# Optimization experiments

Measured on AMD Instinct MI355X. Metric: run time of the kernel, lower is better.

## Reference

```python
import jax, jax.numpy as jnp
import numpy as np

N = 4096

def setup_inputs() -> dict:
    key = jax.random.key(0)
    kA, kB = jax.random.split(key)
    # A and B are upper-triangular inputs, as the module assumes
    A = jnp.triu(jax.random.normal(kA, (N, N), dtype=jnp.float32))
    B = jnp.triu(jax.random.normal(kB, (N, N), dtype=jnp.float32))
    return {"A": A, "B": B}

def reference(A, B):
    # C = triu(A @ B); product of upper-triangular matrices is upper-triangular,
    # the kernel additionally masks the lower triangle of the output.
    return jnp.triu(A @ B)
```

## Files before the change

### kernel.cpp

```cpp
#include <hip/hip_runtime.h>


#define N   4096
#define NB  32
#define BM  128
#define PK  64
#define CH  8
#define NWG 1000
#define RS  72

typedef __attribute__((ext_vector_type(8))) __bf16 bf16x8;
typedef __attribute__((ext_vector_type(4))) float  floatx4;
typedef __attribute__((ext_vector_type(8))) unsigned short ushort8;

__device__ __forceinline__ unsigned short f32_to_bf16_rne(float f) {
    unsigned u = __builtin_bit_cast(unsigned, f);
    unsigned r = u + 0x7fffu + ((u >> 16) & 1u);
    return (unsigned short)(r >> 16);
}

__global__ __launch_bounds__(256)
void prep_kernel(const float* __restrict__ A, const float* __restrict__ B,
                 unsigned short* __restrict__ Ab, unsigned short* __restrict__ Bt,
                 float* __restrict__ C) {
    __shared__ float tile[64][65];
    const int bx = blockIdx.x, by = blockIdx.y;
    const int x0 = bx * 64, y0 = by * 64;
    const int xb = bx >> 1, yb = by >> 1;
    const int t  = threadIdx.x;
    const int tr = t >> 2, tc = (t & 3) * 16;

    if (xb >= yb) {
        const float* src = A + (size_t)(y0 + tr) * N + x0 + tc;
        const float4 v0 = ((const float4*)src)[0];
        const float4 v1 = ((const float4*)src)[1];
        const float4 v2 = ((const float4*)src)[2];
        const float4 v3 = ((const float4*)src)[3];
        ushort8 o0, o1;
        o0[0]=f32_to_bf16_rne(v0.x); o0[1]=f32_to_bf16_rne(v0.y);
        o0[2]=f32_to_bf16_rne(v0.z); o0[3]=f32_to_bf16_rne(v0.w);
        o0[4]=f32_to_bf16_rne(v1.x); o0[5]=f32_to_bf16_rne(v1.y);
        o0[6]=f32_to_bf16_rne(v1.z); o0[7]=f32_to_bf16_rne(v1.w);
        o1[0]=f32_to_bf16_rne(v2.x); o1[1]=f32_to_bf16_rne(v2.y);
        o1[2]=f32_to_bf16_rne(v2.z); o1[3]=f32_to_bf16_rne(v2.w);
        o1[4]=f32_to_bf16_rne(v3.x); o1[5]=f32_to_bf16_rne(v3.y);
        o1[6]=f32_to_bf16_rne(v3.z); o1[7]=f32_to_bf16_rne(v3.w);
        unsigned short* dst = Ab + (size_t)(y0 + tr) * N + x0 + tc;
        ((ushort8*)dst)[0] = o0;
        ((ushort8*)dst)[1] = o1;
    }
    if (xb <= yb) {
        const float* src = B + (size_t)(x0 + tr) * N + y0 + tc;
        const float4 v0 = ((const float4*)src)[0];
        const float4 v1 = ((const float4*)src)[1];
        const float4 v2 = ((const float4*)src)[2];
        const float4 v3 = ((const float4*)src)[3];
        float* d = &tile[tr][tc];
        d[0]=v0.x; d[1]=v0.y; d[2]=v0.z; d[3]=v0.w;
        d[4]=v1.x; d[5]=v1.y; d[6]=v1.z; d[7]=v1.w;
        d[8]=v2.x; d[9]=v2.y; d[10]=v2.z; d[11]=v2.w;
        d[12]=v3.x; d[13]=v3.y; d[14]=v3.z; d[15]=v3.w;
        __syncthreads();
        ushort8 o0, o1;
        #pragma unroll
        for (int i = 0; i < 8; ++i) o0[i] = f32_to_bf16_rne(tile[tc + i][tr]);
        #pragma unroll
        for (int i = 0; i < 8; ++i) o1[i] = f32_to_bf16_rne(tile[tc + 8 + i][tr]);
        unsigned short* dst = Bt + (size_t)(y0 + tr) * N + x0 + tc;
        ((ushort8*)dst)[0] = o0;
        ((ushort8*)dst)[1] = o1;
    }
    if (xb < yb || (xb - yb) >= CH) {
        float4 z = {0.f, 0.f, 0.f, 0.f};
        float* dst = C + (size_t)(y0 + tr) * N + x0 + tc;
        ((float4*)dst)[0] = z; ((float4*)dst)[1] = z;
        ((float4*)dst)[2] = z; ((float4*)dst)[3] = z;
    }
}

__global__ __launch_bounds__(256, 2)
void trimm_kernel(const unsigned short* __restrict__ Ab,
                  const unsigned short* __restrict__ Bt,
                  float* __restrict__ C) {
    __shared__ unsigned short sA[2][BM * RS];
    __shared__ unsigned short sB[2][BM * RS];

    int rem = blockIdx.x;
    int d = 0, per = 1;
    for (int dd = NB - 1; dd >= 0; --dd) {
        const int p   = (dd + CH) / CH;
        const int cnt = (NB - dd) * p;
        if (rem < cnt) { d = dd; per = p; break; }
        rem -= cnt;
    }
    const int tile  = rem / per;
    const int chunk = rem - tile * per;
    const int bi = tile, bj = tile + d;
    const int c    = d + 1;
    const int base = c / per, extra = c - base * per;
    const int kb0  = bi + chunk * base + (chunk < extra ? chunk : extra);
    const int len  = base + (chunk < extra ? 1 : 0);

    const int tid  = threadIdx.x;
    const int w    = tid >> 6;
    const int lane = tid & 63;
    const int quad = lane >> 4;
    const int l15  = lane & 15;

    const int m0 = (w >> 1) * 64;
    const int n0 = (w & 1) * 64;
    const int row0 = bi * BM;
    const int col0 = bj * BM;

    floatx4 acc[4][4] = {};

    const int srow8 = lane >> 3;
    const int sk    = (lane & 7) * 8;
    int lofs[4];
    const unsigned short* gA[4];
    const unsigned short* gB[4];
    #pragma unroll
    for (int i = 0; i < 4; ++i) {
        const int r = w * 32 + i * 8 + srow8;
        lofs[i] = r * RS + sk;
        gA[i] = Ab + (size_t)(row0 + r) * N + kb0 * BM + sk;
        gB[i] = Bt + (size_t)(col0 + r) * N + kb0 * BM + sk;
    }

    const int np = len * 2;

    ushort8 aR[4], bR[4];
    #pragma unroll
    for (int i = 0; i < 4; ++i) { aR[i] = *(const ushort8*)gA[i]; gA[i] += PK; }
    #pragma unroll
    for (int i = 0; i < 4; ++i) { bR[i] = *(const ushort8*)gB[i]; gB[i] += PK; }

    auto compute_phase = [&](int buf) {
        #pragma unroll
        for (int h = 0; h < 2; ++h) {
            bf16x8 af[4], bfr[4];
            #pragma unroll
            for (int t = 0; t < 4; ++t) {
                af[t]  = *(const bf16x8*)&sA[buf][(m0 + t * 16 + l15) * RS + h * 32 + quad * 8];
                bfr[t] = *(const bf16x8*)&sB[buf][(n0 + t * 16 + l15) * RS + h * 32 + quad * 8];
            }
            #pragma unroll
            for (int tm = 0; tm < 4; ++tm)
                #pragma unroll
                for (int tn = 0; tn < 4; ++tn)
                    acc[tm][tn] = __builtin_amdgcn_mfma_f32_16x16x32_bf16(
                        af[tm], bfr[tn], acc[tm][tn], 0, 0, 0);
        }
    };

    for (int p = 0; p < np - 1; ++p) {
        const int buf = p & 1;
        #pragma unroll
        for (int i = 0; i < 4; ++i) *(ushort8*)&sA[buf][lofs[i]] = aR[i];
        #pragma unroll
        for (int i = 0; i < 4; ++i) *(ushort8*)&sB[buf][lofs[i]] = bR[i];
        __syncthreads();
        #pragma unroll
        for (int i = 0; i < 4; ++i) { aR[i] = *(const ushort8*)gA[i]; gA[i] += PK; }
        #pragma unroll
        for (int i = 0; i < 4; ++i) { bR[i] = *(const ushort8*)gB[i]; gB[i] += PK; }
        compute_phase(buf);
    }
    {
        const int buf = (np - 1) & 1;
        #pragma unroll
        for (int i = 0; i < 4; ++i) *(ushort8*)&sA[buf][lofs[i]] = aR[i];
        #pragma unroll
        for (int i = 0; i < 4; ++i) *(ushort8*)&sB[buf][lofs[i]] = bR[i];
        __syncthreads();
        compute_phase(buf);
    }

    #pragma unroll
    for (int tm = 0; tm < 4; ++tm) {
        const int grow_base = row0 + m0 + tm * 16 + quad * 4;
        #pragma unroll
        for (int tn = 0; tn < 4; ++tn) {
            const int gcol = col0 + n0 + tn * 16 + l15;
            #pragma unroll
            for (int r = 0; r < 4; ++r) {
                const int grow = grow_base + r;
                float* p = C + (size_t)grow * N + gcol;
                const float v = acc[tm][tn][r];
                if (per > 1) {
                    atomicAdd(p, v);
                } else if (d != 0) {
                    *p = v;
                } else {
                    *p = (gcol >= grow) ? v : 0.0f;
                }
            }
        }
    }
}

extern "C" void kernel_launch(void* const* d_in, const int* in_sizes, int n_in,
                              void* d_out, int out_size, void* d_ws, size_t ws_size,
                              hipStream_t stream) {
    const float* A = (const float*)d_in[0];
    const float* B = (const float*)d_in[1];
    float* C = (float*)d_out;

    unsigned short* Ab = (unsigned short*)d_ws;
    unsigned short* Bt = Ab + (size_t)N * N;

    prep_kernel<<<dim3(N / 64, N / 64), dim3(256), 0, stream>>>(A, B, Ab, Bt, C);
    trimm_kernel<<<dim3(NWG), dim3(256), 0, stream>>>(Ab, Bt, C);
}
```

Before: 234.7 us.

## Replace split-K atomic scheduling with persistent snake-ordered full-K tile jobs

The kernel no longer splits the K range of long off-diagonal tiles across workgroups with atomicAdd accumulation. Instead it launches 512 persistent workgroups that walk the 528 upper-triangular output tiles in snake order, each computing its full K range and storing results directly. The prep kernel no longer pre-zeroes the output tiles that were accumulated with atomics. This removes the atomic traffic and the extra zeroing, but the longest tiles now run 32 K-blocks serially in a single workgroup, which risks severe load imbalance on the critical path.

```diff
diff --git a/kernel.cpp b/kernel.cpp
--- a/kernel.cpp
+++ b/kernel.cpp
@@ -1,13 +1,13 @@
 #include <hip/hip_runtime.h>
 
 
-#define N   4096
-#define NB  32
-#define BM  128
-#define PK  64
-#define CH  8
-#define NWG 1000
-#define RS  72
+#define N    4096
+#define NB   32
+#define BM   128
+#define PK   64
+#define NWG  512
+#define NJOB 528
+#define RS   72
 
 typedef __attribute__((ext_vector_type(8))) __bf16 bf16x8;
 typedef __attribute__((ext_vector_type(4))) float  floatx4;
@@ -70,7 +70,7 @@
         ((ushort8*)dst)[0] = o0;
         ((ushort8*)dst)[1] = o1;
     }
-    if (xb < yb || (xb - yb) >= CH) {
+    if (xb < yb) {
         float4 z = {0.f, 0.f, 0.f, 0.f};
         float* dst = C + (size_t)(y0 + tr) * N + x0 + tc;
         ((float4*)dst)[0] = z; ((float4*)dst)[1] = z;
@@ -85,22 +85,6 @@
     __shared__ unsigned short sA[2][BM * RS];
     __shared__ unsigned short sB[2][BM * RS];
 
-    int rem = blockIdx.x;
-    int d = 0, per = 1;
-    for (int dd = NB - 1; dd >= 0; --dd) {
-        const int p   = (dd + CH) / CH;
-        const int cnt = (NB - dd) * p;
-        if (rem < cnt) { d = dd; per = p; break; }
-        rem -= cnt;
-    }
-    const int tile  = rem / per;
-    const int chunk = rem - tile * per;
-    const int bi = tile, bj = tile + d;
-    const int c    = d + 1;
-    const int base = c / per, extra = c - base * per;
-    const int kb0  = bi + chunk * base + (chunk < extra ? chunk : extra);
-    const int len  = base + (chunk < extra ? 1 : 0);
-
     const int tid  = threadIdx.x;
     const int w    = tid >> 6;
     const int lane = tid & 63;
@@ -109,90 +93,116 @@
 
     const int m0 = (w >> 1) * 64;
     const int n0 = (w & 1) * 64;
-    const int row0 = bi * BM;
-    const int col0 = bj * BM;
-
-    floatx4 acc[4][4] = {};
 
     const int srow8 = lane >> 3;
     const int sk    = (lane & 7) * 8;
-    int lofs[4];
-    const unsigned short* gA[4];
-    const unsigned short* gB[4];
+    int lofs[4], rr[4];
     #pragma unroll
     for (int i = 0; i < 4; ++i) {
-        const int r = w * 32 + i * 8 + srow8;
-        lofs[i] = r * RS + sk;
-        gA[i] = Ab + (size_t)(row0 + r) * N + kb0 * BM + sk;
-        gB[i] = Bt + (size_t)(col0 + r) * N + kb0 * BM + sk;
-    }
-
-    const int np = len * 2;
-
-    ushort8 aR[4], bR[4];
-    #pragma unroll
-    for (int i = 0; i < 4; ++i) { aR[i] = *(const ushort8*)gA[i]; gA[i] += PK; }
-    #pragma unroll
-    for (int i = 0; i < 4; ++i) { bR[i] = *(const ushort8*)gB[i]; gB[i] += PK; }
-
-    auto compute_phase = [&](int buf) {
-        #pragma unroll
-        for (int h = 0; h < 2; ++h) {
-            bf16x8 af[4], bfr[4];
-            #pragma unroll
-            for (int t = 0; t < 4; ++t) {
-                af[t]  = *(const bf16x8*)&sA[buf][(m0 + t * 16 + l15) * RS + h * 32 + quad * 8];
-                bfr[t] = *(const bf16x8*)&sB[buf][(n0 + t * 16 + l15) * RS + h * 32 + quad * 8];
+        rr[i]   = w * 32 + i * 8 + srow8;
+        lofs[i] = rr[i] * RS + sk;
+    }
+
+    for (int p = 0;; ++p) {
+        const int idx = p * NWG + ((p & 1) ? (NWG - 1 - (int)blockIdx.x)
+                                           : (int)blockIdx.x);
+        if (idx >= NJOB) break;
+
+        int rem = idx, d = NB - 1;
+        for (; d >= 0; --d) {
+            const int cnt = NB - d;
+            if (rem < cnt) break;
+            rem -= cnt;
+        }
+        const int bi = rem, bj = bi + d;
+        const int row0 = bi * BM;
+        const int col0 = bj * BM;
+
+        floatx4 acc[4][4] = {};
+
+        const unsigned short* gA[4];
+        const unsigned short* gB[4];
+        #pragma unroll
+        for (int i = 0; i < 4; ++i) {
+            gA[i] = Ab + (size_t)(row0 + rr[i]) * N + bi * BM + sk;
+            gB[i] = Bt + (size_t)(col0 + rr[i]) * N + bi * BM + sk;
+        }
+
+        const int np = (d + 1) * 2;
+
+        ushort8 aR[4], bR[4];
+        #pragma unroll
+        for (int i = 0; i < 4; ++i) { aR[i] = *(const ushort8*)gA[i]; gA[i] += PK; }
+        #pragma unroll
+        for (int i = 0; i < 4; ++i) { bR[i] = *(const ushort8*)gB[i]; gB[i] += PK; }
+
+        for (int ph = 0; ph < np - 1; ++ph) {
+            const int buf = ph & 1;
+            #pragma unroll
+            for (int i = 0; i < 4; ++i) *(ushort8*)&sA[buf][lofs[i]] = aR[i];
+            #pragma unroll
+            for (int i = 0; i < 4; ++i) *(ushort8*)&sB[buf][lofs[i]] = bR[i];
+            __syncthreads();
+            #pragma unroll
+            for (int i = 0; i < 4; ++i) { aR[i] = *(const ushort8*)gA[i]; gA[i] += PK; }
+            #pragma unroll
+            for (int i = 0; i < 4; ++i) { bR[i] = *(const ushort8*)gB[i]; gB[i] += PK; }
+            #pragma unroll
+            for (int h = 0; h < 2; ++h) {
+                bf16x8 af[4], bfr[4];
+                #pragma unroll
+                for (int t = 0; t < 4; ++t) {
+                    af[t]  = *(const bf16x8*)&sA[buf][(m0 + t * 16 + l15) * RS + h * 32 + quad * 8];
+                    bfr[t] = *(const bf16x8*)&sB[buf][(n0 + t * 16 + l15) * RS + h * 32 + quad * 8];
+                }
+                #pragma unroll
+                for (int tm = 0; tm < 4; ++tm)
+                    #pragma unroll
+                    for (int tn = 0; tn < 4; ++tn)
+                        acc[tm][tn] = __builtin_amdgcn_mfma_f32_16x16x32_bf16(
+                            af[tm], bfr[tn], acc[tm][tn], 0, 0, 0);
             }
-            #pragma unroll
-            for (int tm = 0; tm < 4; ++tm)
-                #pragma unroll
-                for (int tn = 0; tn < 4; ++tn)
-                    acc[tm][tn] = __builtin_amdgcn_mfma_f32_16x16x32_bf16(
-                        af[tm], bfr[tn], acc[tm][tn], 0, 0, 0);
-        }
-    };
-
-    for (int p = 0; p < np - 1; ++p) {
-        const int buf = p & 1;
-        #pragma unroll
-        for (int i = 0; i < 4; ++i) *(ushort8*)&sA[buf][lofs[i]] = aR[i];
-        #pragma unroll
-        for (int i = 0; i < 4; ++i) *(ushort8*)&sB[buf][lofs[i]] = bR[i];
-        __syncthreads();
-        #pragma unroll
-        for (int i = 0; i < 4; ++i) { aR[i] = *(const ushort8*)gA[i]; gA[i] += PK; }
-        #pragma unroll
-        for (int i = 0; i < 4; ++i) { bR[i] = *(const ushort8*)gB[i]; gB[i] += PK; }
-        compute_phase(buf);
-    }
-    {
-        const int buf = (np - 1) & 1;
-        #pragma unroll
-        for (int i = 0; i < 4; ++i) *(ushort8*)&sA[buf][lofs[i]] = aR[i];
-        #pragma unroll
-        for (int i = 0; i < 4; ++i) *(ushort8*)&sB[buf][lofs[i]] = bR[i];
-        __syncthreads();
-        compute_phase(buf);
-    }
-
-    #pragma unroll
-    for (int tm = 0; tm < 4; ++tm) {
-        const int grow_base = row0 + m0 + tm * 16 + quad * 4;
-        #pragma unroll
-        for (int tn = 0; tn < 4; ++tn) {
-            const int gcol = col0 + n0 + tn * 16 + l15;
-            #pragma unroll
-            for (int r = 0; r < 4; ++r) {
-                const int grow = grow_base + r;
-                float* p = C + (size_t)grow * N + gcol;
-                const float v = acc[tm][tn][r];
-                if (per > 1) {
-                    atomicAdd(p, v);
-                } else if (d != 0) {
-                    *p = v;
-                } else {
-                    *p = (gcol >= grow) ? v : 0.0f;
+        }
+        {
+            const int buf = (np - 1) & 1;
+            #pragma unroll
+            for (int i = 0; i < 4; ++i) *(ushort8*)&sA[buf][lofs[i]] = aR[i];
+            #pragma unroll
+            for (int i = 0; i < 4; ++i) *(ushort8*)&sB[buf][lofs[i]] = bR[i];
+            __syncthreads();
+            #pragma unroll
+            for (int h = 0; h < 2; ++h) {
+                bf16x8 af[4], bfr[4];
+                #pragma unroll
+                for (int t = 0; t < 4; ++t) {
+                    af[t]  = *(const bf16x8*)&sA[buf][(m0 + t * 16 + l15) * RS + h * 32 + quad * 8];
+                    bfr[t] = *(const bf16x8*)&sB[buf][(n0 + t * 16 + l15) * RS + h * 32 + quad * 8];
+                }
+                #pragma unroll
+                for (int tm = 0; tm < 4; ++tm)
+                    #pragma unroll
+                    for (int tn = 0; tn < 4; ++tn)
+                        acc[tm][tn] = __builtin_amdgcn_mfma_f32_16x16x32_bf16(
+                            af[tm], bfr[tn], acc[tm][tn], 0, 0, 0);
+            }
+            __syncthreads();
+        }
+
+        #pragma unroll
+        for (int tm = 0; tm < 4; ++tm) {
+            const int grow_base = row0 + m0 + tm * 16 + quad * 4;
+            #pragma unroll
+            for (int tn = 0; tn < 4; ++tn) {
+                const int gcol = col0 + n0 + tn * 16 + l15;
+                #pragma unroll
+                for (int r = 0; r < 4; ++r) {
+                    const int grow = grow_base + r;
+                    const float v = acc[tm][tn][r];
+                    if (d != 0) {
+                        C[(size_t)grow * N + gcol] = v;
+                    } else {
+                        C[(size_t)grow * N + gcol] = (gcol >= grow) ? v : 0.0f;
+                    }
                 }
             }
         }
```

Result: faster. 229.7 us (-2.1%).
